# Optimization experiments

Measured on AMD Instinct MI355X. Metric: run time of the kernel, lower is better.

## Reference

```python
import jax, jax.numpy as jnp
import numpy as np

H = 20   # hidden_size
L = 5    # num_layers


def _gru_layer(x_seq, W_ih, W_hh, b_ih, b_hh):
    """x_seq: [T, B, in]. Returns (hs [T,B,H], h_last [B,H]). PyTorch GRU math."""
    T, B, _ = x_seq.shape
    # precompute input projections for all timesteps: [T, B, 3H]
    x_proj = jnp.einsum('tbi,gi->tbg', x_seq, W_ih) + b_ih
    h0 = jnp.zeros((B, H), x_seq.dtype)

    def step(h, xp):
        gh = h @ W_hh.T + b_hh                      # [B, 3H]
        xr, xz, xn = jnp.split(xp, 3, axis=-1)
        hr, hz, hn = jnp.split(gh, 3, axis=-1)
        r = jax.nn.sigmoid(xr + hr)
        z = jax.nn.sigmoid(xz + hz)
        n = jnp.tanh(xn + r * hn)
        h_new = (1.0 - z) * n + z * h
        return h_new, h_new

    h_last, hs = jax.lax.scan(step, h0, x_proj)
    return hs, h_last


def setup_inputs() -> dict:
    key = jax.random.key(0)
    ks = jax.random.split(key, 1 + 4 * L + 2)
    B, T = 256, 4096
    s = 1.0 / np.sqrt(H)  # torch RNN default init bound
    inp = {"x": jax.random.normal(ks[0], (B, T, 1), jnp.float32)}
    i = 1
    for l in range(L):
        in_sz = 1 if l == 0 else H
        inp[f"W_ih_{l}"] = jax.random.uniform(ks[i], (3 * H, in_sz), jnp.float32, -s, s); i += 1
        inp[f"W_hh_{l}"] = jax.random.uniform(ks[i], (3 * H, H), jnp.float32, -s, s); i += 1
        inp[f"b_ih_{l}"] = jax.random.uniform(ks[i], (3 * H,), jnp.float32, -s, s); i += 1
        inp[f"b_hh_{l}"] = jax.random.uniform(ks[i], (3 * H,), jnp.float32, -s, s); i += 1
    s2 = 1.0 / np.sqrt(L * H)
    inp["W_out"] = jax.random.uniform(ks[i], (1, L * H), jnp.float32, -s2, s2)
    inp["b_out"] = jax.random.uniform(ks[i + 1], (1,), jnp.float32, -s2, s2)
    return inp


def reference(x,
              W_ih_0, W_hh_0, b_ih_0, b_hh_0,
              W_ih_1, W_hh_1, b_ih_1, b_hh_1,
              W_ih_2, W_hh_2, b_ih_2, b_hh_2,
              W_ih_3, W_hh_3, b_ih_3, b_hh_3,
              W_ih_4, W_hh_4, b_ih_4, b_hh_4,
              W_out, b_out):
    Wih = [W_ih_0, W_ih_1, W_ih_2, W_ih_3, W_ih_4]
    Whh = [W_hh_0, W_hh_1, W_hh_2, W_hh_3, W_hh_4]
    bih = [b_ih_0, b_ih_1, b_ih_2, b_ih_3, b_ih_4]
    bhh = [b_hh_0, b_hh_1, b_hh_2, b_hh_3, b_hh_4]

    seq = jnp.transpose(x, (1, 0, 2))  # [T, B, 1] (torch x.transpose(1,0))
    h_lasts = []
    for l in range(L):
        seq, h_last = _gru_layer(seq, Wih[l], Whh[l], bih[l], bhh[l])
        h_lasts.append(h_last)

    h = jnp.transpose(seq, (1, 0, 2))          # [B, T, H] last-layer outputs
    h_n = jnp.stack(h_lasts, axis=1)           # [B, L, H]
    y_hat = h_n.reshape(h_n.shape[0], -1) @ W_out.T + b_out  # [B, 1]
    return h, h_n, y_hat
```

## Files before the change

### kernel.cpp

```cpp
#include <hip/hip_runtime.h>


#define HH 20
#define GG 60
#define NL 5
#define BB 256
#define TT 4096
#define KK 16
#define NC (TT / KK)
#define RD 4

typedef float f4 __attribute__((ext_vector_type(4)));

struct Params {
  const float* x;
  const float* wih[NL];
  const float* whh[NL];
  const float* bih[NL];
  const float* bhh[NL];
  const float* wout;
  const float* bout;
  float* out;
};

__device__ __forceinline__ float bcast_dyn(float v, int j) {
  return __int_as_float(__builtin_amdgcn_readlane(__float_as_int(v), j));
}
__device__ __forceinline__ float shfl_idx(float v, int byteidx) {
  return __int_as_float(__builtin_amdgcn_ds_bpermute(byteidx, __float_as_int(v)));
}
__device__ __forceinline__ float ftanh_s(float ys) {
  return fmaf(2.0f, __builtin_amdgcn_rcpf(1.0f + __builtin_amdgcn_exp2f(ys)), -1.0f);
}
__device__ __forceinline__ int ldv(const int* p) {
  return *(const volatile int*)p;
}

__global__ __launch_bounds__(NL * 64, 1) void gru5_kernel(Params p) {
  __shared__ float xring[NL - 1][RD][KK + 1][64];
  __shared__ __align__(16) float hbuf[NL][64];
  __shared__ float yp[NL];
  __shared__ int prog[NL - 1];
  __shared__ int cons[NL - 1];

  const int tid = threadIdx.x;
  const int l = tid >> 6;
  const int lane = tid & 63;
  const int b = blockIdx.x;
  const int g = lane < GG ? lane : GG - 1;
  const int gn = lane < HH ? lane + 2 * HH : GG - 1;

  if (tid < NL - 1) { prog[tid] = 0; cons[tid] = 0; }

  const float S1 = -1.44269504088896f;
  const float S2 = -2.88539008177793f;
  const float scg = (g < 2 * HH) ? S1 : S2;

  f4 whh4[5];
  {
    const float* W = p.whh[l];
    #pragma unroll
    for (int k = 0; k < 5; ++k) {
      whh4[k].x = W[g * HH + 4 * k]     * scg;
      whh4[k].y = W[g * HH + 4 * k + 1] * scg;
      whh4[k].z = W[g * HH + 4 * k + 2] * scg;
      whh4[k].w = W[g * HH + 4 * k + 3] * scg;
    }
  }
  const float binit = (g >= 2 * HH) ? p.bhh[l][g] * S2 : 0.0f;

  f4 wnx4[5];
  float bnx = 0.0f;
  if (l < NL - 1) {
    const float* W = p.wih[l + 1];
    #pragma unroll
    for (int k = 0; k < 5; ++k) {
      wnx4[k].x = W[g * HH + 4 * k]     * scg;
      wnx4[k].y = W[g * HH + 4 * k + 1] * scg;
      wnx4[k].z = W[g * HH + 4 * k + 2] * scg;
      wnx4[k].w = W[g * HH + 4 * k + 3] * scg;
    }
    bnx = (p.bih[l + 1][g] + (g < 2 * HH ? p.bhh[l + 1][g] : 0.0f)) * scg;
  } else {
    #pragma unroll
    for (int k = 0; k < 5; ++k) { wnx4[k].x = 0.f; wnx4[k].y = 0.f; wnx4[k].z = 0.f; wnx4[k].w = 0.f; }
  }
  float w0own = 0.f, b0own = 0.f, w0n = 0.f, b0n = 0.f;
  if (l == 0) {
    w0own = p.wih[0][g] * scg;
    b0own = (p.bih[0][g] + (g < 2 * HH ? p.bhh[0][g] : 0.0f)) * scg;
    w0n = p.wih[0][gn] * S2;
    b0n = p.bih[0][gn] * S2;
  }

  const int idx20 = ((lane + 20) & 63) << 2;
  const int idx40 = ((lane + 40) & 63) << 2;

  float hreg = 0.0f;
  f4 hq[5];
  #pragma unroll
  for (int k = 0; k < 5; ++k) { hq[k].x = 0.f; hq[k].y = 0.f; hq[k].z = 0.f; hq[k].w = 0.f; }

  const float* xrow = p.x + (size_t)b * TT;
  float* hout = p.out + (size_t)b * TT * HH;

  auto matvec = [&]() -> float {
    f4 a; a.x = binit; a.y = 0.f; a.z = 0.f; a.w = 0.f;
    #pragma unroll
    for (int k = 0; k < 5; ++k) a = __builtin_elementwise_fma(whh4[k], hq[k], a);
    return (a.x + a.z) + (a.y + a.w);
  };
  auto refresh_hs = [&]() {
    hbuf[l][lane] = hreg;
    asm volatile("" ::: "memory");
    const f4* hv = (const f4*)&hbuf[l][0];
    hq[0] = hv[0]; hq[1] = hv[1]; hq[2] = hv[2]; hq[3] = hv[3]; hq[4] = hv[4];
  };
  auto proj = [&]() -> float {
    f4 c; c.x = bnx; c.y = 0.f; c.z = 0.f; c.w = 0.f;
    #pragma unroll
    for (int k = 0; k < 5; ++k) c = __builtin_elementwise_fma(wnx4[k], hq[k], c);
    return (c.x + c.z) + (c.y + c.w);
  };

  __syncthreads();

  float xstage = 0.0f;
  if (l == 0 && lane < KK) xstage = xrow[lane];

  for (int c = 0; c < NC; ++c) {
    if (l > 0) {
      while (ldv(&prog[l - 1]) < c + 1) __builtin_amdgcn_s_sleep(1);
    }
    if (l < NL - 1) {
      while (ldv(&cons[l]) < c + 1 - RD) __builtin_amdgcn_s_sleep(1);
    }

    if (l == 0) {
      float* dst = &xring[0][c & (RD - 1)][0][0];
      float xnl = 0.0f;
      if (lane < KK && c + 1 < NC) xnl = xrow[(c + 1) * KK + lane];
      #pragma unroll 4
      for (int t = 0; t < KK; ++t) {
        const float xv = bcast_dyn(xstage, t);
        const float xr = fmaf(w0own, xv, b0own);
        const float xn = fmaf(w0n, xv, b0n);
        const float gh = matvec();
        const float sv = xr + gh;
        const float sg = __builtin_amdgcn_rcpf(1.0f + __builtin_amdgcn_exp2f(sv));
        const float zf = shfl_idx(sg, idx20);
        const float ghn = shfl_idx(gh, idx40);
        if (t > 0) dst[(t - 1) * 64 + lane] = proj();
        const float n = ftanh_s(fmaf(sg, ghn, xn));
        hreg = fmaf(zf, hreg - n, n);
        refresh_hs();
      }
      dst[(KK - 1) * 64 + lane] = proj();
      xstage = xnl;
    } else if (l < NL - 1) {
      const float* src = &xring[l - 1][c & (RD - 1)][0][0];
      float* dst = &xring[l][c & (RD - 1)][0][0];
      float xr_c = src[g];
      float xn_c = src[gn];
      #pragma unroll 4
      for (int t = 0; t < KK; ++t) {
        const float* nsrc = src + (t + 1) * 64;
        const float xr_n = nsrc[g];
        const float xn_n = nsrc[gn];
        const float gh = matvec();
        const float sv = xr_c + gh;
        const float sg = __builtin_amdgcn_rcpf(1.0f + __builtin_amdgcn_exp2f(sv));
        const float zf = shfl_idx(sg, idx20);
        const float ghn = shfl_idx(gh, idx40);
        if (t > 0) dst[(t - 1) * 64 + lane] = proj();
        const float n = ftanh_s(fmaf(sg, ghn, xn_c));
        hreg = fmaf(zf, hreg - n, n);
        refresh_hs();
        xr_c = xr_n; xn_c = xn_n;
      }
      dst[(KK - 1) * 64 + lane] = proj();
    } else {
      const float* src = &xring[NL - 2][c & (RD - 1)][0][0];
      float* hp = hout + (size_t)c * KK * HH;
      float xr_c = src[g];
      float xn_c = src[gn];
      #pragma unroll 4
      for (int t = 0; t < KK; ++t) {
        const float* nsrc = src + (t + 1) * 64;
        const float xr_n = nsrc[g];
        const float xn_n = nsrc[gn];
        const float gh = matvec();
        const float sv = xr_c + gh;
        const float sg = __builtin_amdgcn_rcpf(1.0f + __builtin_amdgcn_exp2f(sv));
        const float zf = shfl_idx(sg, idx20);
        const float ghn = shfl_idx(gh, idx40);
        if (t > 0 && lane < HH) hp[(t - 1) * HH + lane] = hreg;
        const float n = ftanh_s(fmaf(sg, ghn, xn_c));
        hreg = fmaf(zf, hreg - n, n);
        refresh_hs();
        xr_c = xr_n; xn_c = xn_n;
      }
      if (lane < HH) hp[(KK - 1) * HH + lane] = hreg;
    }

    if (l < NL - 1) {
      __threadfence_block();
      if (lane == 0) *(volatile int*)&prog[l] = c + 1;
    }
    if (l > 0) {
      if (lane == 0) *(volatile int*)&cons[l - 1] = c + 1;
    }
  }

  if (lane < HH)
    p.out[(size_t)BB * TT * HH + (size_t)b * NL * HH + l * HH + lane] = hreg;
  float pp = (lane < HH) ? hreg * p.wout[l * HH + lane] : 0.0f;
  #pragma unroll
  for (int off = 32; off > 0; off >>= 1) pp += __shfl_down(pp, off);
  if (lane == 0) yp[l] = pp;

  __syncthreads();
  if (tid == 0) {
    float y = p.bout[0];
    #pragma unroll
    for (int ll = 0; ll < NL; ++ll) y += yp[ll];
    p.out[(size_t)BB * TT * HH + (size_t)BB * NL * HH + b] = y;
  }
}

extern "C" void kernel_launch(void* const* d_in, const int* in_sizes, int n_in,
                              void* d_out, int out_size, void* d_ws, size_t ws_size,
                              hipStream_t stream) {
  Params p;
  p.x = (const float*)d_in[0];
  for (int l = 0; l < NL; ++l) {
    p.wih[l] = (const float*)d_in[1 + 4 * l];
    p.whh[l] = (const float*)d_in[2 + 4 * l];
    p.bih[l] = (const float*)d_in[3 + 4 * l];
    p.bhh[l] = (const float*)d_in[4 + 4 * l];
  }
  p.wout = (const float*)d_in[1 + 4 * NL];
  p.bout = (const float*)d_in[2 + 4 * NL];
  p.out = (float*)d_out;

  gru5_kernel<<<BB, NL * 64, 0, stream>>>(p);
}
```

Before: 907.0 us.

## Compute all three gate matvecs per hidden lane, removing cross-lane permutes

```diff
diff --git a/kernel.cpp b/kernel.cpp
--- a/kernel.cpp
+++ b/kernel.cpp
@@ -26,8 +26,8 @@
 __device__ __forceinline__ float bcast_dyn(float v, int j) {
   return __int_as_float(__builtin_amdgcn_readlane(__float_as_int(v), j));
 }
-__device__ __forceinline__ float shfl_idx(float v, int byteidx) {
-  return __int_as_float(__builtin_amdgcn_ds_bpermute(byteidx, __float_as_int(v)));
+__device__ __forceinline__ float fsig_s(float xs) {
+  return __builtin_amdgcn_rcpf(1.0f + __builtin_amdgcn_exp2f(xs));
 }
 __device__ __forceinline__ float ftanh_s(float ys) {
   return fmaf(2.0f, __builtin_amdgcn_rcpf(1.0f + __builtin_amdgcn_exp2f(ys)), -1.0f);
@@ -38,7 +38,7 @@
 
 __global__ __launch_bounds__(NL * 64, 1) void gru5_kernel(Params p) {
   __shared__ float xring[NL - 1][RD][KK + 1][64];
-  __shared__ __align__(16) float hbuf[NL][64];
+  __shared__ __align__(16) float hbuf[NL][32];
   __shared__ float yp[NL];
   __shared__ int prog[NL - 1];
   __shared__ int cons[NL - 1];
@@ -48,7 +48,7 @@
   const int lane = tid & 63;
   const int b = blockIdx.x;
   const int g = lane < GG ? lane : GG - 1;
-  const int gn = lane < HH ? lane + 2 * HH : GG - 1;
+  const int u = lane < HH ? lane : HH - 1;
 
   if (tid < NL - 1) { prog[tid] = 0; cons[tid] = 0; }
 
@@ -56,18 +56,23 @@
   const float S2 = -2.88539008177793f;
   const float scg = (g < 2 * HH) ? S1 : S2;
 
-  f4 whh4[5];
+  f4 wr4[5], wz4[5], wn4[5];
   {
     const float* W = p.whh[l];
+    const float* Wr = W + (size_t)u * HH;
+    const float* Wz = W + (size_t)(u + HH) * HH;
+    const float* Wn = W + (size_t)(u + 2 * HH) * HH;
     #pragma unroll
     for (int k = 0; k < 5; ++k) {
-      whh4[k].x = W[g * HH + 4 * k]     * scg;
-      whh4[k].y = W[g * HH + 4 * k + 1] * scg;
-      whh4[k].z = W[g * HH + 4 * k + 2] * scg;
-      whh4[k].w = W[g * HH + 4 * k + 3] * scg;
-    }
-  }
-  const float binit = (g >= 2 * HH) ? p.bhh[l][g] * S2 : 0.0f;
+      wr4[k].x = Wr[4 * k] * S1;  wr4[k].y = Wr[4 * k + 1] * S1;
+      wr4[k].z = Wr[4 * k + 2] * S1;  wr4[k].w = Wr[4 * k + 3] * S1;
+      wz4[k].x = Wz[4 * k] * S1;  wz4[k].y = Wz[4 * k + 1] * S1;
+      wz4[k].z = Wz[4 * k + 2] * S1;  wz4[k].w = Wz[4 * k + 3] * S1;
+      wn4[k].x = Wn[4 * k] * S2;  wn4[k].y = Wn[4 * k + 1] * S2;
+      wn4[k].z = Wn[4 * k + 2] * S2;  wn4[k].w = Wn[4 * k + 3] * S2;
+    }
+  }
+  const float bnn = p.bhh[l][u + 2 * HH] * S2;
 
   f4 wnx4[5];
   float bnx = 0.0f;
@@ -85,16 +90,15 @@
     #pragma unroll
     for (int k = 0; k < 5; ++k) { wnx4[k].x = 0.f; wnx4[k].y = 0.f; wnx4[k].z = 0.f; wnx4[k].w = 0.f; }
   }
-  float w0own = 0.f, b0own = 0.f, w0n = 0.f, b0n = 0.f;
+  float w0r = 0.f, b0r = 0.f, w0z = 0.f, b0z = 0.f, w0n = 0.f, b0n = 0.f;
   if (l == 0) {
-    w0own = p.wih[0][g] * scg;
-    b0own = (p.bih[0][g] + (g < 2 * HH ? p.bhh[0][g] : 0.0f)) * scg;
-    w0n = p.wih[0][gn] * S2;
-    b0n = p.bih[0][gn] * S2;
-  }
-
-  const int idx20 = ((lane + 20) & 63) << 2;
-  const int idx40 = ((lane + 40) & 63) << 2;
+    w0r = p.wih[0][u] * S1;
+    b0r = (p.bih[0][u] + p.bhh[0][u]) * S1;
+    w0z = p.wih[0][u + HH] * S1;
+    b0z = (p.bih[0][u + HH] + p.bhh[0][u + HH]) * S1;
+    w0n = p.wih[0][u + 2 * HH] * S2;
+    b0n = p.bih[0][u + 2 * HH] * S2;
+  }
 
   float hreg = 0.0f;
   f4 hq[5];
@@ -104,14 +108,23 @@
   const float* xrow = p.x + (size_t)b * TT;
   float* hout = p.out + (size_t)b * TT * HH;
 
-  auto matvec = [&]() -> float {
-    f4 a; a.x = binit; a.y = 0.f; a.z = 0.f; a.w = 0.f;
-    #pragma unroll
-    for (int k = 0; k < 5; ++k) a = __builtin_elementwise_fma(whh4[k], hq[k], a);
-    return (a.x + a.z) + (a.y + a.w);
+  float ghr, ghz, ghn;
+  auto matvec3 = [&]() {
+    f4 ar; ar.x = 0.f;  ar.y = 0.f; ar.z = 0.f; ar.w = 0.f;
+    f4 az; az.x = 0.f;  az.y = 0.f; az.z = 0.f; az.w = 0.f;
+    f4 an; an.x = bnn;  an.y = 0.f; an.z = 0.f; an.w = 0.f;
+    #pragma unroll
+    for (int k = 0; k < 5; ++k) {
+      ar = __builtin_elementwise_fma(wr4[k], hq[k], ar);
+      az = __builtin_elementwise_fma(wz4[k], hq[k], az);
+      an = __builtin_elementwise_fma(wn4[k], hq[k], an);
+    }
+    ghr = (ar.x + ar.z) + (ar.y + ar.w);
+    ghz = (az.x + az.z) + (az.y + az.w);
+    ghn = (an.x + an.z) + (an.y + an.w);
   };
   auto refresh_hs = [&]() {
-    hbuf[l][lane] = hreg;
+    if (lane < HH) hbuf[l][lane] = hreg;
     asm volatile("" ::: "memory");
     const f4* hv = (const f4*)&hbuf[l][0];
     hq[0] = hv[0]; hq[1] = hv[1]; hq[2] = hv[2]; hq[3] = hv[3]; hq[4] = hv[4];
@@ -121,6 +134,15 @@
     #pragma unroll
     for (int k = 0; k < 5; ++k) c = __builtin_elementwise_fma(wnx4[k], hq[k], c);
     return (c.x + c.z) + (c.y + c.w);
+  };
+  auto gru_step = [&](float xr, float xz, float xn) {
+    matvec3();
+    const float svr = xr + ghr;
+    const float svz = xz + ghz;
+    const float sgr = fsig_s(svr);
+    const float sgz = fsig_s(svz);
+    const float n = ftanh_s(fmaf(sgr, ghn, xn));
+    hreg = fmaf(sgz, hreg - n, n);
   };
 
   __syncthreads();
@@ -140,19 +162,10 @@
       float* dst = &xring[0][c & (RD - 1)][0][0];
       float xnl = 0.0f;
       if (lane < KK && c + 1 < NC) xnl = xrow[(c + 1) * KK + lane];
-      #pragma unroll 4
       for (int t = 0; t < KK; ++t) {
         const float xv = bcast_dyn(xstage, t);
-        const float xr = fmaf(w0own, xv, b0own);
-        const float xn = fmaf(w0n, xv, b0n);
-        const float gh = matvec();
-        const float sv = xr + gh;
-        const float sg = __builtin_amdgcn_rcpf(1.0f + __builtin_amdgcn_exp2f(sv));
-        const float zf = shfl_idx(sg, idx20);
-        const float ghn = shfl_idx(gh, idx40);
         if (t > 0) dst[(t - 1) * 64 + lane] = proj();
-        const float n = ftanh_s(fmaf(sg, ghn, xn));
-        hreg = fmaf(zf, hreg - n, n);
+        gru_step(fmaf(w0r, xv, b0r), fmaf(w0z, xv, b0z), fmaf(w0n, xv, b0n));
         refresh_hs();
       }
       dst[(KK - 1) * 64 + lane] = proj();
@@ -160,45 +173,35 @@
     } else if (l < NL - 1) {
       const float* src = &xring[l - 1][c & (RD - 1)][0][0];
       float* dst = &xring[l][c & (RD - 1)][0][0];
-      float xr_c = src[g];
-      float xn_c = src[gn];
-      #pragma unroll 4
+      float xr_c = src[u];
+      float xz_c = src[u + HH];
+      float xn_c = src[u + 2 * HH];
       for (int t = 0; t < KK; ++t) {
         const float* nsrc = src + (t + 1) * 64;
-        const float xr_n = nsrc[g];
-        const float xn_n = nsrc[gn];
-        const float gh = matvec();
-        const float sv = xr_c + gh;
-        const float sg = __builtin_amdgcn_rcpf(1.0f + __builtin_amdgcn_exp2f(sv));
-        const float zf = shfl_idx(sg, idx20);
-        const float ghn = shfl_idx(gh, idx40);
+        const float xr_n = nsrc[u];
+        const float xz_n = nsrc[u + HH];
+        const float xn_n = nsrc[u + 2 * HH];
         if (t > 0) dst[(t - 1) * 64 + lane] = proj();
-        const float n = ftanh_s(fmaf(sg, ghn, xn_c));
-        hreg = fmaf(zf, hreg - n, n);
+        gru_step(xr_c, xz_c, xn_c);
         refresh_hs();
-        xr_c = xr_n; xn_c = xn_n;
+        xr_c = xr_n; xz_c = xz_n; xn_c = xn_n;
       }
       dst[(KK - 1) * 64 + lane] = proj();
     } else {
       const float* src = &xring[NL - 2][c & (RD - 1)][0][0];
       float* hp = hout + (size_t)c * KK * HH;
-      float xr_c = src[g];
-      float xn_c = src[gn];
-      #pragma unroll 4
+      float xr_c = src[u];
+      float xz_c = src[u + HH];
+      float xn_c = src[u + 2 * HH];
       for (int t = 0; t < KK; ++t) {
         const float* nsrc = src + (t + 1) * 64;
-        const float xr_n = nsrc[g];
-        const float xn_n = nsrc[gn];
-        const float gh = matvec();
-        const float sv = xr_c + gh;
-        const float sg = __builtin_amdgcn_rcpf(1.0f + __builtin_amdgcn_exp2f(sv));
-        const float zf = shfl_idx(sg, idx20);
-        const float ghn = shfl_idx(gh, idx40);
+        const float xr_n = nsrc[u];
+        const float xz_n = nsrc[u + HH];
+        const float xn_n = nsrc[u + 2 * HH];
         if (t > 0 && lane < HH) hp[(t - 1) * HH + lane] = hreg;
-        const float n = ftanh_s(fmaf(sg, ghn, xn_c));
-        hreg = fmaf(zf, hreg - n, n);
+        gru_step(xr_c, xz_c, xn_c);
         refresh_hs();
-        xr_c = xr_n; xn_c = xn_n;
+        xr_c = xr_n; xz_c = xz_n; xn_c = xn_n;
       }
       if (lane < HH) hp[(KK - 1) * HH + lane] = hreg;
     }
```

Result: slower. 1.391 ms (+53.4%).
